# Optimization experiments

Measured on AMD Instinct MI355X. Metric: run time of the kernel, lower is better.

## Reference

```python
import jax, jax.numpy as jnp
import numpy as np

K = 3          # kernel_size
DILATION = 1
STRIDE = 1
B, C_IN, C_OUT, L = 16, 128, 128, 4096
L_OUT = L - DILATION * (K - 1)  # 'valid' padding, stride 1 -> 4094


def setup_inputs() -> dict:
    key = jax.random.key(0)
    k1, k2, k3, k4, k5 = jax.random.split(key, 5)
    x = jax.random.normal(k1, (B, C_IN, L), dtype=jnp.float32)
    offsets = jax.random.normal(k2, (B, 1, L_OUT, K), dtype=jnp.float32)
    mask = jax.random.uniform(k3, (B, K, L_OUT), dtype=jnp.float32)
    weight = jax.random.normal(k4, (C_OUT, C_IN, K), dtype=jnp.float32) * 0.05
    bias = jax.random.normal(k5, (C_OUT,), dtype=jnp.float32) * 0.05
    return {"x": x, "offsets": offsets, "mask": mask, "weight": weight, "bias": bias}


def _deform_conv1d(x, offsets, mask, weight, bias):
    b, c, l = x.shape
    l_out = offsets.shape[-2]
    dtype = offsets.dtype
    # dilated kernel positions: linspace(0, dil*K - dil, K) -> [0, 1, ..., K-1] for dil=1
    dil_pos = jnp.linspace(0.0, DILATION * K - DILATION, K, dtype=dtype)  # [K]
    t0s = (jnp.arange(l_out, dtype=dtype) * STRIDE)[:, None]             # [L_out, 1]
    T = t0s + dil_pos + offsets                                          # [B,1,L_out,K]
    # constrained sampling: keep each kernel's samples within its receptive field
    T = jnp.minimum(jnp.maximum(T, t0s), t0s + dil_pos[-1])
    U = jnp.clip(jnp.floor(T), 0, l - 2).astype(jnp.int32)               # [B,1,L_out,K] (detached)
    # gather left/right neighbors per channel
    idx = jnp.broadcast_to(U.reshape(b, 1, l_out * K), (b, c, l_out * K))
    x0 = jnp.take_along_axis(x, idx, axis=2).reshape(b, c, l_out, K)
    x1 = jnp.take_along_axis(x, idx + 1, axis=2).reshape(b, c, l_out, K)
    Uf = U.astype(dtype)
    G0 = jnp.maximum(0.0, 1.0 - jnp.abs(Uf - T))        # [B,1,L_out,K]
    G1 = jnp.maximum(0.0, 1.0 - jnp.abs(Uf + 1.0 - T))
    xs = G0 * x0 + G1 * x1                              # [B,C,L_out,K]
    # modulation mask: [B,K,L_out] -> [B,1,L_out,K]
    xs = xs * jnp.transpose(mask, (0, 2, 1))[:, None]
    # conv1d with stride == kernel_size over flattened [B,C,L_out*K] == per-position contraction
    out = jnp.einsum('bctk,ock->bot', xs, weight) + bias[None, :, None]
    return out  # [B, C_out, L_out]


def reference(x, offsets, mask, weight, bias):
    return _deform_conv1d(x, offsets, mask, weight, bias)
```

## Files before the change

kernel.cpp:

```cpp
#include <hip/hip_runtime.h>

#define BB 16
#define CI 128
#define CO 128
#define LL 4096
#define LOUT 4094
#define CK 384
#define TT 32
#define NTPB 4
#define STS 72
#define XSS 400

#define LDS_BARRIER() do { \
    asm volatile("s_waitcnt lgkmcnt(0)" ::: "memory"); \
    __builtin_amdgcn_s_barrier(); \
} while (0)

typedef short short8 __attribute__((ext_vector_type(8)));
typedef float floatx4 __attribute__((ext_vector_type(4)));

__device__ __forceinline__ ushort f2bf(float f) {
    union { float f; uint u; } v; v.f = f;
    uint r = v.u + 0x7FFFu + ((v.u >> 16) & 1u);
    return (ushort)(r >> 16);
}
__device__ __forceinline__ uint pk(ushort a, ushort b) {
    return (uint)a | ((uint)b << 16);
}
__device__ __forceinline__ short8 cvt8(floatx4 v0, floatx4 v1) {
    union { uint u[4]; short8 s; } r;
    r.u[0] = pk(f2bf(v0[0]), f2bf(v0[1]));
    r.u[1] = pk(f2bf(v0[2]), f2bf(v0[3]));
    r.u[2] = pk(f2bf(v1[0]), f2bf(v1[1]));
    r.u[3] = pk(f2bf(v1[2]), f2bf(v1[3]));
    return r.s;
}

__global__ __launch_bounds__(256)
void wcvt2_kernel(const float* __restrict__ w, ushort* __restrict__ wbf2) {
    const int i = blockIdx.x * 256 + threadIdx.x;
    const int o = i >> 7, c = i & 127;
    const float w0 = w[i * 3 + 0], w1 = w[i * 3 + 1], w2 = w[i * 3 + 2];
    wbf2[o * CK +       c] = f2bf(w0);
    wbf2[o * CK + 128 + c] = f2bf(w1);
    wbf2[o * CK + 256 + c] = f2bf(w2);
}

__global__ __launch_bounds__(256, 2)
void dconv1d_dbuf_kernel(const float* __restrict__ x,
                         const float* __restrict__ offs,
                         const float* __restrict__ mask,
                         const ushort* __restrict__ wbf2,
                         const float* __restrict__ bias,
                         float* __restrict__ out) {
    __shared__ ushort St[3][TT][STS];
    __shared__ ushort xs[2][TT][XSS];

    const int tid  = threadIdx.x;
    const int lane = tid & 63;
    const int wv   = tid >> 6;
    const int bid  = blockIdx.x;
    const int lb   = (bid & 7) * 64 + (bid >> 3);
    const int b    = lb >> 5;
    const int t0b  = (lb & 31) * (TT * NTPB);

    const int r15   = lane & 15;
    const int acol8 = (lane >> 4) << 3;

    short8 afr[12][2];
#pragma unroll
    for (int ks = 0; ks < 12; ++ks)
#pragma unroll
        for (int mf = 0; mf < 2; ++mf)
            afr[ks][mf] = *(const short8*)
                (wbf2 + (size_t)(wv * 32 + mf * 16 + r15) * CK + ks * 32 + acol8);

    const float* xrow0 = x + ((size_t)b * CI + wv * 32 +      r15) * LL;
    const float* xrow1 = x + ((size_t)b * CI + wv * 32 + 16 + r15) * LL;
    floatx4 c0[2][2], c1[2][2], xn[2][2];
    {
        const int tb0 = t0b + acol8;
        const int tb1 = t0b + 32 + acol8;
        const int tb2 = t0b + 64 + acol8;
        c0[0][0] = *(const floatx4*)(xrow0 + tb0); c0[0][1] = *(const floatx4*)(xrow0 + tb0 + 4);
        c0[1][0] = *(const floatx4*)(xrow1 + tb0); c0[1][1] = *(const floatx4*)(xrow1 + tb0 + 4);
        c1[0][0] = *(const floatx4*)(xrow0 + tb1); c1[0][1] = *(const floatx4*)(xrow0 + tb1 + 4);
        c1[1][0] = *(const floatx4*)(xrow1 + tb1); c1[1][1] = *(const floatx4*)(xrow1 + tb1 + 4);
        xn[0][0] = *(const floatx4*)(xrow0 + tb2); xn[0][1] = *(const floatx4*)(xrow0 + tb2 + 4);
        xn[1][0] = *(const floatx4*)(xrow1 + tb2); xn[1][1] = *(const floatx4*)(xrow1 + tb2 + 4);
    }

    const int ct  = tid & 31;
    const int ck_ = (tid >> 5) < 3 ? (tid >> 5) : 0;
    float of0 = 0.f, mv0 = 0.f, ofc = 0.f, mvc = 0.f, ofn = 0.f, mvn = 0.f;
    if (tid < 96) {
        const int g0 = t0b + ct;
        of0 = offs[((size_t)b * LOUT + g0) * 3 + ck_];
        mv0 = mask[((size_t)b * 3 + ck_) * LOUT + g0];
        const int g1 = t0b + TT + ct;
        if (g1 < LOUT) {
            ofc = offs[((size_t)b * LOUT + g1) * 3 + ck_];
            mvc = mask[((size_t)b * 3 + ck_) * LOUT + g1];
        }
        const int g2 = t0b + 2 * TT + ct;
        if (g2 < LOUT) {
            ofn = offs[((size_t)b * LOUT + g2) * 3 + ck_];
            mvn = mask[((size_t)b * 3 + ck_) * LOUT + g2];
        }
    }

    float bv[2][4];
#pragma unroll
    for (int mf = 0; mf < 2; ++mf)
#pragma unroll
        for (int r = 0; r < 4; ++r)
            bv[mf][r] = bias[wv * 32 + mf * 16 + ((lane >> 4) << 2) + r];

    {
        uint* stz = (uint*)&St[0][0][0];
        for (int i = tid; i < 3 * TT * STS / 2; i += 256) stz[i] = 0;
    }

    short8 axf[2][2];
#pragma unroll
    for (int mf = 0; mf < 2; ++mf) {
        axf[mf][0] = cvt8(c0[mf][0], c0[mf][1]);
        axf[mf][1] = cvt8(c1[mf][0], c1[mf][1]);
    }
    LDS_BARRIER();

#define COEF_TILE(T0, OF, MV) do { \
    if (tid < 96) { \
        const int gt = (T0) + ct; \
        float cc0 = 0.f, cc1 = 0.f, cc2 = 0.f, cc3 = 0.f; \
        if (gt < LOUT) { \
            const float gtf = (float)gt; \
            float T = (gtf + (float)ck_) + (OF); \
            T = fminf(fmaxf(T, gtf), gtf + 2.0f); \
            int U = (int)floorf(T); \
            if (U > LL - 2) U = LL - 2; \
            const float Uf = (float)U; \
            const float G0 = fmaxf(0.f, 1.f - fabsf(Uf - T)) * (MV); \
            const float G1 = fmaxf(0.f, 1.f - fabsf(Uf + 1.f - T)) * (MV); \
            const int d0 = U - gt; \
            cc0 = (d0 == 0) ? G0 : 0.f; \
            cc1 = (d0 == 0) ? G1 : ((d0 == 1) ? G0 : 0.f); \
            cc2 = (d0 == 1) ? G1 : ((d0 == 2) ? G0 : 0.f); \
            cc3 = (d0 == 2) ? G1 : 0.f; \
        } \
        St[ck_][ct][ct + 0] = f2bf(cc0); \
        St[ck_][ct][ct + 1] = f2bf(cc1); \
        St[ck_][ct][ct + 2] = f2bf(cc2); \
        St[ck_][ct][ct + 3] = f2bf(cc3); \
    } \
} while (0)

#define GEMM1_TILE(I) do { \
    _Pragma("unroll") \
    for (int k = 0; k < 3; ++k) { \
        floatx4 a1[2][2]; \
        _Pragma("unroll") \
        for (int mf = 0; mf < 2; ++mf) \
            _Pragma("unroll") \
            for (int nf = 0; nf < 2; ++nf) { \
                floatx4 z = {0.f, 0.f, 0.f, 0.f}; \
                a1[mf][nf] = z; \
            } \
        _Pragma("unroll") \
        for (int ks1 = 0; ks1 < 2; ++ks1) { \
            const short8 bfa = *(const short8*)(&St[k][r15][ks1 * 32 + acol8]); \
            const short8 bfb = *(const short8*)(&St[k][16 + r15][ks1 * 32 + acol8]); \
            _Pragma("unroll") \
            for (int mf = 0; mf < 2; ++mf) { \
                a1[mf][0] = __builtin_amdgcn_mfma_f32_16x16x32_bf16(axf[mf][ks1], bfa, a1[mf][0], 0, 0, 0); \
                a1[mf][1] = __builtin_amdgcn_mfma_f32_16x16x32_bf16(axf[mf][ks1], bfb, a1[mf][1], 0, 0, 0); \
            } \
        } \
        _Pragma("unroll") \
        for (int mf = 0; mf < 2; ++mf) \
            _Pragma("unroll") \
            for (int nf = 0; nf < 2; ++nf) { \
                const int tcol = nf * 16 + r15; \
                const int cb   = wv * 32 + mf * 16 + ((lane >> 4) << 2); \
                uint2 q; \
                q.x = pk(f2bf(a1[mf][nf][0]), f2bf(a1[mf][nf][1])); \
                q.y = pk(f2bf(a1[mf][nf][2]), f2bf(a1[mf][nf][3])); \
                *(uint2*)(&xs[(I) & 1][tcol][k * 128 + cb]) = q; \
            } \
    } \
} while (0)

#define GEMM2_TILE(J) do { \
    const int t0j = t0b + (J) * TT; \
    floatx4 acc[2][2]; \
    _Pragma("unroll") \
    for (int mf = 0; mf < 2; ++mf) \
        _Pragma("unroll") \
        for (int nf = 0; nf < 2; ++nf) { \
            floatx4 z = {0.f, 0.f, 0.f, 0.f}; \
            acc[mf][nf] = z; \
        } \
    _Pragma("unroll") \
    for (int ks = 0; ks < 12; ++ks) { \
        const short8 bf0 = *(const short8*)(&xs[(J) & 1][r15][ks * 32 + acol8]); \
        const short8 bf1 = *(const short8*)(&xs[(J) & 1][16 + r15][ks * 32 + acol8]); \
        _Pragma("unroll") \
        for (int mf = 0; mf < 2; ++mf) { \
            acc[mf][0] = __builtin_amdgcn_mfma_f32_16x16x32_bf16(afr[ks][mf], bf0, acc[mf][0], 0, 0, 0); \
            acc[mf][1] = __builtin_amdgcn_mfma_f32_16x16x32_bf16(afr[ks][mf], bf1, acc[mf][1], 0, 0, 0); \
        } \
    } \
    _Pragma("unroll") \
    for (int mf = 0; mf < 2; ++mf) \
        _Pragma("unroll") \
        for (int r = 0; r < 4; ++r) { \
            const int o = wv * 32 + mf * 16 + ((lane >> 4) << 2) + r; \
            float* orow = out + ((size_t)b * CO + o) * LOUT; \
            _Pragma("unroll") \
            for (int nf = 0; nf < 2; ++nf) { \
                const int gt = t0j + nf * 16 + r15; \
                if (gt < LOUT) orow[gt] = acc[mf][nf][r] + bv[mf][r]; \
            } \
        } \
} while (0)

    COEF_TILE(t0b, of0, mv0);
    LDS_BARRIER();

#pragma unroll 1
    for (int it = 0; it < NTPB; ++it) {
        if (it > 0) GEMM2_TILE(it - 1);
        GEMM1_TILE(it);
        LDS_BARRIER();

        if (it + 1 < NTPB) {
            COEF_TILE(t0b + (it + 1) * TT, ofc, mvc);
            ofc = ofn; mvc = mvn;
            if (it + 3 < NTPB && tid < 96) {
                const int g = t0b + (it + 3) * TT + ct;
                ofn = 0.f; mvn = 0.f;
                if (g < LOUT) {
                    ofn = offs[((size_t)b * LOUT + g) * 3 + ck_];
                    mvn = mask[((size_t)b * 3 + ck_) * LOUT + g];
                }
            }
#pragma unroll
            for (int mf = 0; mf < 2; ++mf) {
                axf[mf][0] = axf[mf][1];
                axf[mf][1] = cvt8(xn[mf][0], xn[mf][1]);
            }
            if (it + 3 <= NTPB) {
                int tb = t0b + (it + 3) * 32 + acol8;
                if (tb > LL - 8) tb = LL - 8;
                xn[0][0] = *(const floatx4*)(xrow0 + tb);
                xn[0][1] = *(const floatx4*)(xrow0 + tb + 4);
                xn[1][0] = *(const floatx4*)(xrow1 + tb);
                xn[1][1] = *(const floatx4*)(xrow1 + tb + 4);
            }
            LDS_BARRIER();
        }
    }

    GEMM2_TILE(NTPB - 1);
}

extern "C" void kernel_launch(void* const* d_in, const int* in_sizes, int n_in,
                              void* d_out, int out_size, void* d_ws, size_t ws_size,
                              hipStream_t stream) {
    const float* x    = (const float*)d_in[0];
    const float* offs = (const float*)d_in[1];
    const float* mask = (const float*)d_in[2];
    const float* w    = (const float*)d_in[3];
    const float* bias = (const float*)d_in[4];
    float* out = (float*)d_out;
    ushort* wbf2 = (ushort*)d_ws;

    wcvt2_kernel<<<dim3(CO * CI / 256), dim3(256), 0, stream>>>(w, wbf2);
    dconv1d_dbuf_kernel<<<dim3(512), dim3(256), 0, stream>>>(
        x, offs, mask, wbf2, bias, out);
}
```

Measured before the change: 33.22 us.

## Split channel work across 8 waves of 16 rows instead of 4 waves of 32

The block grows from 256 to 512 threads, and each wave now owns 16 channel rows instead of 32. This halves the per-thread register footprint for weight fragments, x fragments and accumulators, which should raise occupancy and give more waves to hide MFMA and memory latency. In exchange each wave issues half the MFMAs per LDS fragment load, so operand reuse drops. Barriers now span twice as many waves, and the coefficient stage still uses only 96 threads.

```diff
diff --git a/kernel.cpp b/kernel.cpp
--- a/kernel.cpp
+++ b/kernel.cpp
@@ -46,13 +46,13 @@
     wbf2[o * CK + 256 + c] = f2bf(w2);
 }
 
-__global__ __launch_bounds__(256, 2)
-void dconv1d_dbuf_kernel(const float* __restrict__ x,
-                         const float* __restrict__ offs,
-                         const float* __restrict__ mask,
-                         const ushort* __restrict__ wbf2,
-                         const float* __restrict__ bias,
-                         float* __restrict__ out) {
+__global__ __launch_bounds__(512, 4)
+void dconv1d_merge_kernel(const float* __restrict__ x,
+                          const float* __restrict__ offs,
+                          const float* __restrict__ mask,
+                          const ushort* __restrict__ wbf2,
+                          const float* __restrict__ bias,
+                          float* __restrict__ out) {
     __shared__ ushort St[3][TT][STS];
     __shared__ ushort xs[2][TT][XSS];
 
@@ -66,28 +66,22 @@
 
     const int r15   = lane & 15;
     const int acol8 = (lane >> 4) << 3;
-
-    short8 afr[12][2];
+    const int row16 = wv * 16 + r15;
+
+    short8 afr[12];
 #pragma unroll
     for (int ks = 0; ks < 12; ++ks)
-#pragma unroll
-        for (int mf = 0; mf < 2; ++mf)
-            afr[ks][mf] = *(const short8*)
-                (wbf2 + (size_t)(wv * 32 + mf * 16 + r15) * CK + ks * 32 + acol8);
-
-    const float* xrow0 = x + ((size_t)b * CI + wv * 32 +      r15) * LL;
-    const float* xrow1 = x + ((size_t)b * CI + wv * 32 + 16 + r15) * LL;
-    floatx4 c0[2][2], c1[2][2], xn[2][2];
+        afr[ks] = *(const short8*)(wbf2 + (size_t)row16 * CK + ks * 32 + acol8);
+
+    const float* xrow = x + ((size_t)b * CI + row16) * LL;
+    floatx4 c0[2], c1[2], xn[2];
     {
         const int tb0 = t0b + acol8;
         const int tb1 = t0b + 32 + acol8;
         const int tb2 = t0b + 64 + acol8;
-        c0[0][0] = *(const floatx4*)(xrow0 + tb0); c0[0][1] = *(const floatx4*)(xrow0 + tb0 + 4);
-        c0[1][0] = *(const floatx4*)(xrow1 + tb0); c0[1][1] = *(const floatx4*)(xrow1 + tb0 + 4);
-        c1[0][0] = *(const floatx4*)(xrow0 + tb1); c1[0][1] = *(const floatx4*)(xrow0 + tb1 + 4);
-        c1[1][0] = *(const floatx4*)(xrow1 + tb1); c1[1][1] = *(const floatx4*)(xrow1 + tb1 + 4);
-        xn[0][0] = *(const floatx4*)(xrow0 + tb2); xn[0][1] = *(const floatx4*)(xrow0 + tb2 + 4);
-        xn[1][0] = *(const floatx4*)(xrow1 + tb2); xn[1][1] = *(const floatx4*)(xrow1 + tb2 + 4);
+        c0[0] = *(const floatx4*)(xrow + tb0); c0[1] = *(const floatx4*)(xrow + tb0 + 4);
+        c1[0] = *(const floatx4*)(xrow + tb1); c1[1] = *(const floatx4*)(xrow + tb1 + 4);
+        xn[0] = *(const floatx4*)(xrow + tb2); xn[1] = *(const floatx4*)(xrow + tb2 + 4);
     }
 
     const int ct  = tid & 31;
@@ -109,24 +103,19 @@
         }
     }
 
-    float bv[2][4];
+    float bv[4];
 #pragma unroll
-    for (int mf = 0; mf < 2; ++mf)
-#pragma unroll
-        for (int r = 0; r < 4; ++r)
-            bv[mf][r] = bias[wv * 32 + mf * 16 + ((lane >> 4) << 2) + r];
+    for (int r = 0; r < 4; ++r)
+        bv[r] = bias[wv * 16 + ((lane >> 4) << 2) + r];
 
     {
         uint* stz = (uint*)&St[0][0][0];
-        for (int i = tid; i < 3 * TT * STS / 2; i += 256) stz[i] = 0;
-    }
-
-    short8 axf[2][2];
-#pragma unroll
-    for (int mf = 0; mf < 2; ++mf) {
-        axf[mf][0] = cvt8(c0[mf][0], c0[mf][1]);
-        axf[mf][1] = cvt8(c1[mf][0], c1[mf][1]);
-    }
+        for (int i = tid; i < 3 * TT * STS / 2; i += 512) stz[i] = 0;
+    }
+
+    short8 axf[2];
+    axf[0] = cvt8(c0[0], c0[1]);
+    axf[1] = cvt8(c1[0], c1[1]);
     LDS_BARRIER();
 
 #define COEF_TILE(T0, OF, MV) do { \
@@ -158,70 +147,56 @@
 #define GEMM1_TILE(I) do { \
     _Pragma("unroll") \
     for (int k = 0; k < 3; ++k) { \
-        floatx4 a1[2][2]; \
-        _Pragma("unroll") \
-        for (int mf = 0; mf < 2; ++mf) \
-            _Pragma("unroll") \
-            for (int nf = 0; nf < 2; ++nf) { \
-                floatx4 z = {0.f, 0.f, 0.f, 0.f}; \
-                a1[mf][nf] = z; \
-            } \
+        floatx4 a1[2]; \
+        _Pragma("unroll") \
+        for (int nf = 0; nf < 2; ++nf) { \
+            floatx4 z = {0.f, 0.f, 0.f, 0.f}; \
+            a1[nf] = z; \
+        } \
         _Pragma("unroll") \
         for (int ks1 = 0; ks1 < 2; ++ks1) { \
             const short8 bfa = *(const short8*)(&St[k][r15][ks1 * 32 + acol8]); \
             const short8 bfb = *(const short8*)(&St[k][16 + r15][ks1 * 32 + acol8]); \
-            _Pragma("unroll") \
-            for (int mf = 0; mf < 2; ++mf) { \
-                a1[mf][0] = __builtin_amdgcn_mfma_f32_16x16x32_bf16(axf[mf][ks1], bfa, a1[mf][0], 0, 0, 0); \
-                a1[mf][1] = __builtin_amdgcn_mfma_f32_16x16x32_bf16(axf[mf][ks1], bfb, a1[mf][1], 0, 0, 0); \
-            } \
-        } \
-        _Pragma("unroll") \
-        for (int mf = 0; mf < 2; ++mf) \
-            _Pragma("unroll") \
-            for (int nf = 0; nf < 2; ++nf) { \
-                const int tcol = nf * 16 + r15; \
-                const int cb   = wv * 32 + mf * 16 + ((lane >> 4) << 2); \
-                uint2 q; \
-                q.x = pk(f2bf(a1[mf][nf][0]), f2bf(a1[mf][nf][1])); \
-                q.y = pk(f2bf(a1[mf][nf][2]), f2bf(a1[mf][nf][3])); \
-                *(uint2*)(&xs[(I) & 1][tcol][k * 128 + cb]) = q; \
-            } \
+            a1[0] = __builtin_amdgcn_mfma_f32_16x16x32_bf16(axf[ks1], bfa, a1[0], 0, 0, 0); \
+            a1[1] = __builtin_amdgcn_mfma_f32_16x16x32_bf16(axf[ks1], bfb, a1[1], 0, 0, 0); \
+        } \
+        _Pragma("unroll") \
+        for (int nf = 0; nf < 2; ++nf) { \
+            const int tcol = nf * 16 + r15; \
+            const int cb   = wv * 16 + ((lane >> 4) << 2); \
+            uint2 q; \
+            q.x = pk(f2bf(a1[nf][0]), f2bf(a1[nf][1])); \
+            q.y = pk(f2bf(a1[nf][2]), f2bf(a1[nf][3])); \
+            *(uint2*)(&xs[(I) & 1][tcol][k * 128 + cb]) = q; \
+        } \
     } \
 } while (0)
 
 #define GEMM2_TILE(J) do { \
     const int t0j = t0b + (J) * TT; \
-    floatx4 acc[2][2]; \
-    _Pragma("unroll") \
-    for (int mf = 0; mf < 2; ++mf) \
-        _Pragma("unroll") \
-        for (int nf = 0; nf < 2; ++nf) { \
-            floatx4 z = {0.f, 0.f, 0.f, 0.f}; \
-            acc[mf][nf] = z; \
-        } \
+    floatx4 acc[2]; \
+    _Pragma("unroll") \
+    for (int nf = 0; nf < 2; ++nf) { \
+        floatx4 z = {0.f, 0.f, 0.f, 0.f}; \
+        acc[nf] = z; \
+    } \
     _Pragma("unroll") \
     for (int ks = 0; ks < 12; ++ks) { \
         const short8 bf0 = *(const short8*)(&xs[(J) & 1][r15][ks * 32 + acol8]); \
         const short8 bf1 = *(const short8*)(&xs[(J) & 1][16 + r15][ks * 32 + acol8]); \
-        _Pragma("unroll") \
-        for (int mf = 0; mf < 2; ++mf) { \
-            acc[mf][0] = __builtin_amdgcn_mfma_f32_16x16x32_bf16(afr[ks][mf], bf0, acc[mf][0], 0, 0, 0); \
-            acc[mf][1] = __builtin_amdgcn_mfma_f32_16x16x32_bf16(afr[ks][mf], bf1, acc[mf][1], 0, 0, 0); \
-        } \
-    } \
-    _Pragma("unroll") \
-    for (int mf = 0; mf < 2; ++mf) \
-        _Pragma("unroll") \
-        for (int r = 0; r < 4; ++r) { \
-            const int o = wv * 32 + mf * 16 + ((lane >> 4) << 2) + r; \
-            float* orow = out + ((size_t)b * CO + o) * LOUT; \
-            _Pragma("unroll") \
-            for (int nf = 0; nf < 2; ++nf) { \
-                const int gt = t0j + nf * 16 + r15; \
-                if (gt < LOUT) orow[gt] = acc[mf][nf][r] + bv[mf][r]; \
-            } \
-        } \
+        acc[0] = __builtin_amdgcn_mfma_f32_16x16x32_bf16(afr[ks], bf0, acc[0], 0, 0, 0); \
+        acc[1] = __builtin_amdgcn_mfma_f32_16x16x32_bf16(afr[ks], bf1, acc[1], 0, 0, 0); \
+    } \
+    _Pragma("unroll") \
+    for (int r = 0; r < 4; ++r) { \
+        const int o = wv * 16 + ((lane >> 4) << 2) + r; \
+        float* orow = out + ((size_t)b * CO + o) * LOUT; \
+        _Pragma("unroll") \
+        for (int nf = 0; nf < 2; ++nf) { \
+            const int gt = t0j + nf * 16 + r15; \
+            if (gt < LOUT) orow[gt] = acc[nf][r] + bv[r]; \
+        } \
+    } \
 } while (0)
 
     COEF_TILE(t0b, of0, mv0);
@@ -244,18 +219,13 @@
                     mvn = mask[((size_t)b * 3 + ck_) * LOUT + g];
                 }
             }
-#pragma unroll
-            for (int mf = 0; mf < 2; ++mf) {
-                axf[mf][0] = axf[mf][1];
-                axf[mf][1] = cvt8(xn[mf][0], xn[mf][1]);
-            }
+            axf[0] = axf[1];
+            axf[1] = cvt8(xn[0], xn[1]);
             if (it + 3 <= NTPB) {
                 int tb = t0b + (it + 3) * 32 + acol8;
                 if (tb > LL - 8) tb = LL - 8;
-                xn[0][0] = *(const floatx4*)(xrow0 + tb);
-                xn[0][1] = *(const floatx4*)(xrow0 + tb + 4);
-                xn[1][0] = *(const floatx4*)(xrow1 + tb);
-                xn[1][1] = *(const floatx4*)(xrow1 + tb + 4);
+                xn[0] = *(const floatx4*)(xrow + tb);
+                xn[1] = *(const floatx4*)(xrow + tb + 4);
             }
             LDS_BARRIER();
         }
@@ -276,6 +246,6 @@
     ushort* wbf2 = (ushort*)d_ws;
 
     wcvt2_kernel<<<dim3(CO * CI / 256), dim3(256), 0, stream>>>(w, wbf2);
-    dconv1d_dbuf_kernel<<<dim3(512), dim3(256), 0, stream>>>(
+    dconv1d_merge_kernel<<<dim3(512), dim3(512), 0, stream>>>(
         x, offs, mask, wbf2, bias, out);
 }
```

Measured after the change: 32.70 us, median of 2. About the same (-1.6%).
